# Performance work log

Hardware: AMD Instinct MI355X
Metric: run time of the kernel (lower is better)

Reference implementation:

```python
import jax, jax.numpy as jnp
import numpy as np
from jax import lax

B, C, H, W, D, V = 1, 32, 128, 160, 64, 5


def _make_projs():
    # proj_matrices[b, v, 0] = 4x4 extrinsics [R|t], proj_matrices[b, v, 1] = 4x4 intrinsics
    f = 800.0
    K = np.eye(4, dtype=np.float32)
    K[0, 0] = K[1, 1] = f
    K[0, 2] = W / 2.0
    K[1, 2] = H / 2.0
    projs = np.zeros((B, V, 2, 4, 4), np.float32)
    for b in range(B):
        for v in range(V):
            E = np.eye(4, dtype=np.float32)
            if v > 0:
                ang = 0.02 * v
                ca, sa = np.cos(ang), np.sin(ang)
                E[:3, :3] = np.array([[ca, 0.0, sa], [0.0, 1.0, 0.0], [-sa, 0.0, ca]], np.float32)
                E[:3, 3] = np.array([0.1 * v, 0.02 * v, 0.05 * v], np.float32)
            projs[b, v, 0] = E
            projs[b, v, 1] = K
    return jnp.asarray(projs)


def setup_inputs() -> dict:
    key = jax.random.key(0)
    ks = jax.random.split(key, 6)
    inp = {f"feat{i}": jax.random.normal(ks[i], (B, C, H, W), jnp.float32) for i in range(V)}
    inp["proj_matrices"] = _make_projs()
    inp["depth_values"] = jnp.broadcast_to(
        jnp.linspace(425.0, 935.0, D, dtype=jnp.float32)[None, :], (B, D))
    inp["num_depth"] = D
    inp["conv_w"] = jax.random.normal(ks[5], (1, C, 3, 3, 3), jnp.float32) * 0.05
    inp["conv_b"] = jnp.zeros((1,), jnp.float32)
    return inp


def _bilinear_sample(fea, px, py):
    # fea: [B,C,H,W]; px,py: [B,N] pixel coords. Bilinear, zero padding, align_corners=True.
    Bb, Cc, Hh, Ww = fea.shape
    fea_flat = fea.reshape(Bb, Cc, Hh * Ww)
    x0 = jnp.floor(px)
    y0 = jnp.floor(py)
    wx1 = px - x0
    wy1 = py - y0

    def corner(xc, yc, w):
        valid = (xc >= 0) & (xc <= Ww - 1) & (yc >= 0) & (yc <= Hh - 1)
        xi = jnp.clip(xc, 0, Ww - 1).astype(jnp.int32)
        yi = jnp.clip(yc, 0, Hh - 1).astype(jnp.int32)
        idx = yi * Ww + xi  # [B,N]
        g = jax.vmap(lambda fb, ib: fb[:, ib])(fea_flat, idx)  # [B,C,N]
        return g * (w * valid)[:, None, :]

    return (corner(x0, y0, (1 - wx1) * (1 - wy1))
            + corner(x0 + 1, y0, wx1 * (1 - wy1))
            + corner(x0, y0 + 1, (1 - wx1) * wy1)
            + corner(x0 + 1, y0 + 1, wx1 * wy1))


def _homo_warp(src_fea, src_proj, ref_proj, depth_values):
    # homo_warping_3D: warp src features into ref frustum at each depth hypothesis
    Bb, Cc, Hh, Ww = src_fea.shape
    Dd = depth_values.shape[1]
    proj = jnp.einsum('bij,bjk->bik', src_proj, jnp.linalg.inv(ref_proj))
    rot, trans = proj[:, :3, :3], proj[:, :3, 3]
    yy, xx = jnp.meshgrid(jnp.arange(Hh, dtype=src_fea.dtype),
                          jnp.arange(Ww, dtype=src_fea.dtype), indexing='ij')
    xyz = jnp.stack([xx.ravel(), yy.ravel(), jnp.ones(Hh * Ww, src_fea.dtype)])  # [3,HW]
    rot_xyz = jnp.einsum('bij,jn->bin', rot, xyz)  # [B,3,HW]
    pxyz = rot_xyz[:, :, None, :] * depth_values[:, None, :, None] + trans[:, :, None, None]  # [B,3,D,HW]
    px = (pxyz[:, 0] / pxyz[:, 2]).reshape(Bb, -1)
    py = (pxyz[:, 1] / pxyz[:, 2]).reshape(Bb, -1)
    return _bilinear_sample(src_fea, px, py).reshape(Bb, Cc, Dd, Hh, Ww)


def _fuse_proj(p):
    # p: [B,2,4,4] -> [B,4,4] with K[:3,:3] @ E[:3,:4] written into top 3 rows
    top = jnp.einsum('bij,bjk->bik', p[:, 1, :3, :3], p[:, 0, :3, :4])
    return p[:, 0].at[:, :3, :4].set(top)


def reference(feat0, feat1, feat2, feat3, feat4, proj_matrices, depth_values, num_depth, conv_w, conv_b):
    feats = [feat0, feat1, feat2, feat3, feat4]
    num_views = len(feats)
    Bb, Cc, Hh, Ww = feat0.shape
    ref_proj = _fuse_proj(proj_matrices[:, 0])
    ref_vol = jnp.broadcast_to(feat0[:, :, None, :, :], (Bb, Cc, num_depth, Hh, Ww))
    vol_sum = ref_vol
    vol_sq = ref_vol ** 2
    for v in range(1, num_views):
        src_proj = _fuse_proj(proj_matrices[:, v])
        warped = _homo_warp(feats[v], src_proj, ref_proj, depth_values)
        vol_sum = vol_sum + warped
        vol_sq = vol_sq + warped ** 2
    variance = vol_sq / num_views - (vol_sum / num_views) ** 2  # [B,C,D,H,W]
    cost = lax.conv_general_dilated(variance, conv_w, (1, 1, 1), 'SAME',
                                    dimension_numbers=('NCDHW', 'OIDHW', 'NCDHW'))
    cost = cost + conv_b[None, :, None, None, None]
    prob_volume_pre = cost[:, 0]  # squeeze channel -> [B,D,H,W]
    return jax.nn.softmax(prob_volume_pre, axis=1)
```

## Files before the change

### kernel.cpp

```cpp
#include <hip/hip_runtime.h>

#define H_ 128
#define W_ 160
#define C_ 32
#define D_ 64
#define HW_ (H_*W_)
#define DHW_ (D_*HW_)
#define NVIEW 5

#define TY 16
#define TX 16
#define HY 18
#define HXP 19
#define NP_ (HY*HXP)
#define PSTR 343

#define FEATT_SZ (NVIEW*HW_*C_)
#define MATS_OFF FEATT_SZ
#define A_OFF (MATS_OFF + 64)

__global__ void k_setup_mats(const float* __restrict__ proj,
                             float* __restrict__ mats)
{
    if (threadIdx.x != 0 || blockIdx.x != 0) return;
    double F[5][12];
    for (int v = 0; v < 5; ++v) {
        const float* E = proj + v*32;
        const float* K = proj + v*32 + 16;
        for (int i = 0; i < 3; ++i)
            for (int j = 0; j < 4; ++j) {
                double s = 0.0;
                for (int k = 0; k < 3; ++k)
                    s += (double)K[i*4+k] * (double)E[k*4+j];
                F[v][i*4+j] = s;
            }
    }
    const double m00=F[0][0], m01=F[0][1], m02=F[0][2],  t0x=F[0][3];
    const double m10=F[0][4], m11=F[0][5], m12=F[0][6],  t0y=F[0][7];
    const double m20=F[0][8], m21=F[0][9], m22=F[0][10], t0z=F[0][11];
    const double det = m00*(m11*m22-m12*m21) - m01*(m10*m22-m12*m20)
                     + m02*(m10*m21-m11*m20);
    const double id = 1.0/det;
    double inv[9];
    inv[0] = (m11*m22-m12*m21)*id; inv[1] = (m02*m21-m01*m22)*id; inv[2] = (m01*m12-m02*m11)*id;
    inv[3] = (m12*m20-m10*m22)*id; inv[4] = (m00*m22-m02*m20)*id; inv[5] = (m02*m10-m00*m12)*id;
    inv[6] = (m10*m21-m11*m20)*id; inv[7] = (m01*m20-m00*m21)*id; inv[8] = (m00*m11-m01*m10)*id;
    double it[3];
    it[0] = -(inv[0]*t0x + inv[1]*t0y + inv[2]*t0z);
    it[1] = -(inv[3]*t0x + inv[4]*t0y + inv[5]*t0z);
    it[2] = -(inv[6]*t0x + inv[7]*t0y + inv[8]*t0z);
    for (int v = 1; v < 5; ++v) {
        float* o = mats + (v-1)*12;
        for (int r = 0; r < 3; ++r) {
            for (int c = 0; c < 3; ++c) {
                double s = 0.0;
                for (int k = 0; k < 3; ++k) s += F[v][r*4+k]*inv[k*3+c];
                o[r*3+c] = (float)s;
            }
            double tr = F[v][r*4+3] + F[v][r*4+0]*it[0]
                      + F[v][r*4+1]*it[1] + F[v][r*4+2]*it[2];
            o[9+r] = (float)tr;
        }
    }
}

__global__ void k_transpose(const float* __restrict__ f, float* __restrict__ ft)
{
    __shared__ float tile[C_][65];
    const int pix0 = blockIdx.x * 64;
    const int tid = threadIdx.x;
    const int p  = tid & 63;
    const int ci = (tid >> 6) * 8;
#pragma unroll
    for (int i = 0; i < 8; ++i)
        tile[ci + i][p] = f[(size_t)(ci + i)*HW_ + pix0 + p];
    __syncthreads();
    const int c2 = tid & 31, pg = tid >> 5;
#pragma unroll
    for (int i = 0; i < 8; ++i) {
        int p2 = pg + i*8;
        ft[(size_t)(pix0 + p2)*C_ + c2] = tile[c2][p2];
    }
}

__global__ __launch_bounds__(256, 3) void k_var_conv(
    const float* __restrict__ featT, const float* __restrict__ mats,
    const float* __restrict__ depthv, const float* __restrict__ convw,
    float* __restrict__ A)
{
    __shared__ float var_lds[C_ * PSTR];
    const int x0 = blockIdx.x * TX;
    const int y0 = blockIdx.y * TY;
    const int bd = blockIdx.z;
    const float depth = depthv[bd];

    float cf[4][9];
#pragma unroll
    for (int v = 0; v < 4; ++v) {
        const float* mm = mats + v*12;
#pragma unroll
        for (int r = 0; r < 3; ++r) {
            cf[v][r*3+0] = mm[r*3+0]*depth;
            cf[v][r*3+1] = mm[r*3+1]*depth;
            cf[v][r*3+2] = fmaf(mm[r*3+2], depth, mm[9+r]);
        }
    }

    const int lane_c = (threadIdx.x & 7) * 4;
    const int pg     = threadIdx.x >> 3;

    for (int p = pg; p < NP_; p += 32) {
        const int hy = p / HXP;
        const int hx = p - hy*HXP;
        const int gy = y0 - 1 + hy;
        const int gx = x0 - 1 + hx;
        float var[4] = {0.f, 0.f, 0.f, 0.f};
        if (hx < (TX+2) && (unsigned)gy < (unsigned)H_ && (unsigned)gx < (unsigned)W_) {
            const float fgx = (float)gx, fgy = (float)gy;
            const int pix = gy*W_ + gx;
            float s[4], q[4];
            {
                float4 t = *reinterpret_cast<const float4*>(featT + (size_t)pix*C_ + lane_c);
                s[0]=t.x; s[1]=t.y; s[2]=t.z; s[3]=t.w;
#pragma unroll
                for (int k = 0; k < 4; ++k) q[k] = s[k]*s[k];
            }
#pragma unroll
            for (int v = 0; v < 4; ++v) {
                const float xx = fmaf(cf[v][0],fgx, fmaf(cf[v][1],fgy, cf[v][2]));
                const float yy = fmaf(cf[v][3],fgx, fmaf(cf[v][4],fgy, cf[v][5]));
                const float zz = fmaf(cf[v][6],fgx, fmaf(cf[v][7],fgy, cf[v][8]));
                const float rz = 1.0f / zz;
                const float px = xx*rz, py = yy*rz;
                const float xf = floorf(px), yf = floorf(py);
                const float wx = px - xf, wy = py - yf;
                const int xi = (int)xf, yi = (int)yf;
                const bool vx0 = (xi >=  0) & (xi <= W_-1);
                const bool vx1 = (xi >= -1) & (xi <= W_-2);
                const bool vy0 = (yi >=  0) & (yi <= H_-1);
                const bool vy1 = (yi >= -1) & (yi <= H_-2);
                const int xc0 = min(max(xi,   0), W_-1);
                const int xc1 = min(max(xi+1, 0), W_-1);
                const int yc0 = min(max(yi,   0), H_-1);
                const int yc1 = min(max(yi+1, 0), H_-1);
                const float ux = 1.f - wx, uy = 1.f - wy;
                const float w00 = (vx0 && vy0) ? ux*uy : 0.f;
                const float w10 = (vx1 && vy0) ? wx*uy : 0.f;
                const float w01 = (vx0 && vy1) ? ux*wy : 0.f;
                const float w11 = (vx1 && vy1) ? wx*wy : 0.f;
                const float* fb = featT + (size_t)(v+1)*HW_*C_ + lane_c;
                const float4 t00 = *reinterpret_cast<const float4*>(fb + (size_t)(yc0*W_+xc0)*C_);
                const float4 t10 = *reinterpret_cast<const float4*>(fb + (size_t)(yc0*W_+xc1)*C_);
                const float4 t01 = *reinterpret_cast<const float4*>(fb + (size_t)(yc1*W_+xc0)*C_);
                const float4 t11 = *reinterpret_cast<const float4*>(fb + (size_t)(yc1*W_+xc1)*C_);
                const float a00[4] = {t00.x,t00.y,t00.z,t00.w};
                const float a10[4] = {t10.x,t10.y,t10.z,t10.w};
                const float a01[4] = {t01.x,t01.y,t01.z,t01.w};
                const float a11[4] = {t11.x,t11.y,t11.z,t11.w};
#pragma unroll
                for (int k = 0; k < 4; ++k) {
                    float wv = fmaf(a00[k],w00, fmaf(a10[k],w10, fmaf(a01[k],w01, a11[k]*w11)));
                    s[k] += wv;
                    q[k] = fmaf(wv, wv, q[k]);
                }
            }
#pragma unroll
            for (int k = 0; k < 4; ++k) {
                const float sm = s[k]*0.2f;
                var[k] = q[k]*0.2f - sm*sm;
            }
        }
#pragma unroll
        for (int k = 0; k < 4; ++k)
            var_lds[(lane_c+k)*PSTR + p] = var[k];
    }
    __syncthreads();

    const int tid = threadIdx.x;
    const int oy = tid >> 4;
    const int ox = tid & 15;
    float a0 = 0.f, a1 = 0.f, a2 = 0.f;
#pragma unroll 4
    for (int cc = 0; cc < C_; ++cc) {
        const float* vrow = var_lds + cc*PSTR;
        const float* wc   = convw + cc*27;
#pragma unroll
        for (int ky = 0; ky < 3; ++ky) {
            const int base = (oy+ky)*HXP + ox;
            const float u0 = vrow[base+0];
            const float u1 = vrow[base+1];
            const float u2 = vrow[base+2];
            const float* wk = wc + ky*3;
            a0 = fmaf(u0, wk[0],  fmaf(u1, wk[1],  fmaf(u2, wk[2],  a0)));
            a1 = fmaf(u0, wk[9],  fmaf(u1, wk[10], fmaf(u2, wk[11], a1)));
            a2 = fmaf(u0, wk[18], fmaf(u1, wk[19], fmaf(u2, wk[20], a2)));
        }
    }
    const size_t o = (size_t)bd*HW_ + (size_t)(y0+oy)*W_ + (x0+ox);
    A[o]                    = a0;
    A[(size_t)DHW_ + o]     = a1;
    A[2*(size_t)DHW_ + o]   = a2;
}

__global__ void k_softmax(const float* __restrict__ A,
                          const float* __restrict__ conv_b,
                          float* __restrict__ out)
{
    const int pix = blockIdx.x*256 + threadIdx.x;
    const float bs = conv_b[0];
    float cst[D_];
#pragma unroll
    for (int d = 0; d < D_; ++d) {
        float v = A[(size_t)DHW_ + (size_t)d*HW_ + pix];
        if (d > 0)      v += A[(size_t)(d-1)*HW_ + pix];
        if (d < D_-1)   v += A[2*(size_t)DHW_ + (size_t)(d+1)*HW_ + pix];
        cst[d] = v + bs;
    }
    float m = cst[0];
#pragma unroll
    for (int d = 1; d < D_; ++d) m = fmaxf(m, cst[d]);
    float s = 0.f;
#pragma unroll
    for (int d = 0; d < D_; ++d) { cst[d] = expf(cst[d] - m); s += cst[d]; }
    const float rs = 1.0f / s;
#pragma unroll
    for (int d = 0; d < D_; ++d)
        out[(size_t)d*HW_ + pix] = cst[d]*rs;
}

extern "C" void kernel_launch(void* const* d_in, const int* in_sizes, int n_in,
                              void* d_out, int out_size, void* d_ws, size_t ws_size,
                              hipStream_t stream)
{
    const float* proj   = (const float*)d_in[5];
    const float* depth  = (const float*)d_in[6];
    const float* conv_w = (const float*)d_in[8];
    const float* conv_b = (const float*)d_in[9];

    float* ws    = (float*)d_ws;
    float* featT = ws;
    float* mats  = ws + MATS_OFF;
    float* A     = ws + A_OFF;

    k_setup_mats<<<1, 64, 0, stream>>>(proj, mats);
    for (int v = 0; v < 5; ++v)
        k_transpose<<<HW_/64, 256, 0, stream>>>((const float*)d_in[v],
                                                featT + (size_t)v*HW_*C_);
    dim3 g1(W_/TX, H_/TY, D_);
    k_var_conv<<<g1, 256, 0, stream>>>(featT, mats, depth, conv_w, A);
    k_softmax<<<HW_/256, 256, 0, stream>>>(A, conv_b, (float*)d_out);
}
```

Before: 202.8 us.

## Compute each halo pixel per thread across all channels with swizzled pixel-major LDS

The variance stage now assigns one halo pixel per thread instead of splitting channels across 8 lanes. Each thread computes projection, weights and offsets once per view and loops over all 32 channels, so the homography math is no longer repeated per channel group. The variance tile is stored pixel-major in LDS with an XOR swizzle and read as float4 in the conv stage, using conv weights pre-permuted per tap. The five transpose launches are merged into one 2D grid, and the reciprocal uses the hardware rcp. In exchange, only 324 of 256×2 thread slots do work (about 68 of 256 threads idle on the second pass), register use per thread grows, and each thread's gathers are now uncoalesced 128-byte rows.

```diff
diff --git a/kernel.cpp b/kernel.cpp
--- a/kernel.cpp
+++ b/kernel.cpp
@@ -6,23 +6,31 @@
 #define D_ 64
 #define HW_ (H_*W_)
 #define DHW_ (D_*HW_)
-#define NVIEW 5
 
 #define TY 16
 #define TX 16
-#define HY 18
-#define HXP 19
-#define NP_ (HY*HXP)
-#define PSTR 343
-
-#define FEATT_SZ (NVIEW*HW_*C_)
+#define HS 18
+#define NP_ (HS*HS)
+
+#define FEATT_SZ (5*HW_*C_)
 #define MATS_OFF FEATT_SZ
-#define A_OFF (MATS_OFF + 64)
-
-__global__ void k_setup_mats(const float* __restrict__ proj,
-                             float* __restrict__ mats)
-{
-    if (threadIdx.x != 0 || blockIdx.x != 0) return;
+#define CW2_OFF (MATS_OFF + 64)
+#define A_OFF (CW2_OFF + 960)
+
+__global__ void k_setup(const float* __restrict__ proj,
+                        const float* __restrict__ convw,
+                        float* __restrict__ mats,
+                        float* __restrict__ cw2)
+{
+    const int tid = threadIdx.x;
+    for (int i = tid; i < 864; i += 64) {
+        const int tap = i / 96;
+        const int rem = i - tap*96;
+        const int c   = rem / 3;
+        const int kd  = rem - c*3;
+        cw2[i] = convw[c*27 + kd*9 + tap];
+    }
+    if (tid != 0) return;
     double F[5][12];
     for (int v = 0; v < 5; ++v) {
         const float* E = proj + v*32;
@@ -64,8 +72,13 @@
     }
 }
 
-__global__ void k_transpose(const float* __restrict__ f, float* __restrict__ ft)
-{
+__global__ void k_transpose(const float* __restrict__ f0, const float* __restrict__ f1,
+                            const float* __restrict__ f2, const float* __restrict__ f3,
+                            const float* __restrict__ f4, float* __restrict__ ft)
+{
+    const int bv = blockIdx.y;
+    const float* f = (bv==0) ? f0 : (bv==1) ? f1 : (bv==2) ? f2 : (bv==3) ? f3 : f4;
+    float* o = ft + (size_t)bv * (HW_*C_);
     __shared__ float tile[C_][65];
     const int pix0 = blockIdx.x * 64;
     const int tid = threadIdx.x;
@@ -79,16 +92,17 @@
 #pragma unroll
     for (int i = 0; i < 8; ++i) {
         int p2 = pg + i*8;
-        ft[(size_t)(pix0 + p2)*C_ + c2] = tile[c2][p2];
+        o[(size_t)(pix0 + p2)*C_ + c2] = tile[c2][p2];
     }
 }
 
 __global__ __launch_bounds__(256, 3) void k_var_conv(
     const float* __restrict__ featT, const float* __restrict__ mats,
-    const float* __restrict__ depthv, const float* __restrict__ convw,
+    const float* __restrict__ depthv, const float* __restrict__ cw2,
     float* __restrict__ A)
 {
-    __shared__ float var_lds[C_ * PSTR];
+    __shared__ float vlds[NP_ * C_];
+    const int tid = threadIdx.x;
     const int x0 = blockIdx.x * TX;
     const int y0 = blockIdx.y * TY;
     const int bd = blockIdx.z;
@@ -106,100 +120,133 @@
         }
     }
 
-    const int lane_c = (threadIdx.x & 7) * 4;
-    const int pg     = threadIdx.x >> 3;
-
-    for (int p = pg; p < NP_; p += 32) {
-        const int hy = p / HXP;
-        const int hx = p - hy*HXP;
+    for (int p = tid; p < NP_; p += 256) {
+        const int hy = p / HS;
+        const int hx = p - hy*HS;
         const int gy = y0 - 1 + hy;
         const int gx = x0 - 1 + hx;
-        float var[4] = {0.f, 0.f, 0.f, 0.f};
-        if (hx < (TX+2) && (unsigned)gy < (unsigned)H_ && (unsigned)gx < (unsigned)W_) {
-            const float fgx = (float)gx, fgy = (float)gy;
-            const int pix = gy*W_ + gx;
-            float s[4], q[4];
+        const bool inimg = ((unsigned)gy < 128u) && ((unsigned)gx < 160u);
+        const float vp = inimg ? 1.f : 0.f;
+        const float fgx = (float)gx, fgy = (float)gy;
+        const int gyc = min(max(gy, 0), H_-1);
+        const int gxc = min(max(gx, 0), W_-1);
+        const int refoff = (gyc*W_ + gxc)*C_;
+
+        float wgt[4][4];
+        int   off[4][4];
+#pragma unroll
+        for (int v = 0; v < 4; ++v) {
+            const float xx = fmaf(cf[v][0],fgx, fmaf(cf[v][1],fgy, cf[v][2]));
+            const float yy = fmaf(cf[v][3],fgx, fmaf(cf[v][4],fgy, cf[v][5]));
+            const float zz = fmaf(cf[v][6],fgx, fmaf(cf[v][7],fgy, cf[v][8]));
+            const float rz = __builtin_amdgcn_rcpf(zz);
+            const float px = xx*rz, py = yy*rz;
+            const float xf = floorf(px), yf = floorf(py);
+            const float wx = px - xf, wy = py - yf;
+            const int xi = (int)xf, yi = (int)yf;
+            const bool vx0 = (xi >=  0) & (xi <= W_-1);
+            const bool vx1 = (xi >= -1) & (xi <= W_-2);
+            const bool vy0 = (yi >=  0) & (yi <= H_-1);
+            const bool vy1 = (yi >= -1) & (yi <= H_-2);
+            const int xc0 = min(max(xi,   0), W_-1);
+            const int xc1 = min(max(xi+1, 0), W_-1);
+            const int yr0 = min(max(yi,   0), H_-1) * W_;
+            const int yr1 = min(max(yi+1, 0), H_-1) * W_;
+            const float ux = 1.f - wx, uy = 1.f - wy;
+            wgt[v][0] = (inimg && vx0 && vy0) ? ux*uy : 0.f;
+            wgt[v][1] = (inimg && vx1 && vy0) ? wx*uy : 0.f;
+            wgt[v][2] = (inimg && vx0 && vy1) ? ux*wy : 0.f;
+            wgt[v][3] = (inimg && vx1 && vy1) ? wx*wy : 0.f;
+            off[v][0] = (yr0 + xc0)*C_;
+            off[v][1] = (yr0 + xc1)*C_;
+            off[v][2] = (yr1 + xc0)*C_;
+            off[v][3] = (yr1 + xc1)*C_;
+        }
+
+        const int sw = p & 7;
+        float* vout = vlds + p*C_;
+#pragma unroll
+        for (int cp = 0; cp < 4; ++cp) {
+            const int c0 = cp*8;
+            float s0[4], q0[4], s1[4], q1[4];
             {
-                float4 t = *reinterpret_cast<const float4*>(featT + (size_t)pix*C_ + lane_c);
-                s[0]=t.x; s[1]=t.y; s[2]=t.z; s[3]=t.w;
-#pragma unroll
-                for (int k = 0; k < 4; ++k) q[k] = s[k]*s[k];
+                const float4 t0 = *reinterpret_cast<const float4*>(featT + refoff + c0);
+                const float4 t1 = *reinterpret_cast<const float4*>(featT + refoff + c0 + 4);
+                const float t0a[4] = {t0.x,t0.y,t0.z,t0.w};
+                const float t1a[4] = {t1.x,t1.y,t1.z,t1.w};
+#pragma unroll
+                for (int k = 0; k < 4; ++k) {
+                    s0[k] = t0a[k]*vp;  q0[k] = s0[k]*t0a[k];
+                    s1[k] = t1a[k]*vp;  q1[k] = s1[k]*t1a[k];
+                }
             }
 #pragma unroll
             for (int v = 0; v < 4; ++v) {
-                const float xx = fmaf(cf[v][0],fgx, fmaf(cf[v][1],fgy, cf[v][2]));
-                const float yy = fmaf(cf[v][3],fgx, fmaf(cf[v][4],fgy, cf[v][5]));
-                const float zz = fmaf(cf[v][6],fgx, fmaf(cf[v][7],fgy, cf[v][8]));
-                const float rz = 1.0f / zz;
-                const float px = xx*rz, py = yy*rz;
-                const float xf = floorf(px), yf = floorf(py);
-                const float wx = px - xf, wy = py - yf;
-                const int xi = (int)xf, yi = (int)yf;
-                const bool vx0 = (xi >=  0) & (xi <= W_-1);
-                const bool vx1 = (xi >= -1) & (xi <= W_-2);
-                const bool vy0 = (yi >=  0) & (yi <= H_-1);
-                const bool vy1 = (yi >= -1) & (yi <= H_-2);
-                const int xc0 = min(max(xi,   0), W_-1);
-                const int xc1 = min(max(xi+1, 0), W_-1);
-                const int yc0 = min(max(yi,   0), H_-1);
-                const int yc1 = min(max(yi+1, 0), H_-1);
-                const float ux = 1.f - wx, uy = 1.f - wy;
-                const float w00 = (vx0 && vy0) ? ux*uy : 0.f;
-                const float w10 = (vx1 && vy0) ? wx*uy : 0.f;
-                const float w01 = (vx0 && vy1) ? ux*wy : 0.f;
-                const float w11 = (vx1 && vy1) ? wx*wy : 0.f;
-                const float* fb = featT + (size_t)(v+1)*HW_*C_ + lane_c;
-                const float4 t00 = *reinterpret_cast<const float4*>(fb + (size_t)(yc0*W_+xc0)*C_);
-                const float4 t10 = *reinterpret_cast<const float4*>(fb + (size_t)(yc0*W_+xc1)*C_);
-                const float4 t01 = *reinterpret_cast<const float4*>(fb + (size_t)(yc1*W_+xc0)*C_);
-                const float4 t11 = *reinterpret_cast<const float4*>(fb + (size_t)(yc1*W_+xc1)*C_);
-                const float a00[4] = {t00.x,t00.y,t00.z,t00.w};
-                const float a10[4] = {t10.x,t10.y,t10.z,t10.w};
-                const float a01[4] = {t01.x,t01.y,t01.z,t01.w};
-                const float a11[4] = {t11.x,t11.y,t11.z,t11.w};
+                const float* fb = featT + (size_t)(v+1)*(HW_*C_) + c0;
+                float4 a0c[4], a1c[4];
+#pragma unroll
+                for (int c4 = 0; c4 < 4; ++c4) {
+                    a0c[c4] = *reinterpret_cast<const float4*>(fb + off[v][c4]);
+                    a1c[c4] = *reinterpret_cast<const float4*>(fb + off[v][c4] + 4);
+                }
+                const float w0 = wgt[v][0], w1 = wgt[v][1], w2 = wgt[v][2], w3 = wgt[v][3];
+                const float a00[4]={a0c[0].x,a0c[0].y,a0c[0].z,a0c[0].w};
+                const float a10[4]={a0c[1].x,a0c[1].y,a0c[1].z,a0c[1].w};
+                const float a01[4]={a0c[2].x,a0c[2].y,a0c[2].z,a0c[2].w};
+                const float a11[4]={a0c[3].x,a0c[3].y,a0c[3].z,a0c[3].w};
+                const float b00[4]={a1c[0].x,a1c[0].y,a1c[0].z,a1c[0].w};
+                const float b10[4]={a1c[1].x,a1c[1].y,a1c[1].z,a1c[1].w};
+                const float b01[4]={a1c[2].x,a1c[2].y,a1c[2].z,a1c[2].w};
+                const float b11[4]={a1c[3].x,a1c[3].y,a1c[3].z,a1c[3].w};
 #pragma unroll
                 for (int k = 0; k < 4; ++k) {
-                    float wv = fmaf(a00[k],w00, fmaf(a10[k],w10, fmaf(a01[k],w01, a11[k]*w11)));
-                    s[k] += wv;
-                    q[k] = fmaf(wv, wv, q[k]);
+                    const float wv0 = fmaf(a00[k],w0, fmaf(a10[k],w1, fmaf(a01[k],w2, a11[k]*w3)));
+                    s0[k] += wv0;  q0[k] = fmaf(wv0, wv0, q0[k]);
+                    const float wv1 = fmaf(b00[k],w0, fmaf(b10[k],w1, fmaf(b01[k],w2, b11[k]*w3)));
+                    s1[k] += wv1;  q1[k] = fmaf(wv1, wv1, q1[k]);
                 }
             }
+            float o0[4], o1[4];
 #pragma unroll
             for (int k = 0; k < 4; ++k) {
-                const float sm = s[k]*0.2f;
-                var[k] = q[k]*0.2f - sm*sm;
-            }
-        }
-#pragma unroll
-        for (int k = 0; k < 4; ++k)
-            var_lds[(lane_c+k)*PSTR + p] = var[k];
+                const float m0 = s0[k]*0.2f;  o0[k] = q0[k]*0.2f - m0*m0;
+                const float m1 = s1[k]*0.2f;  o1[k] = q1[k]*0.2f - m1*m1;
+            }
+            *reinterpret_cast<float4*>(vout + (((2*cp  )^sw)<<2)) = make_float4(o0[0],o0[1],o0[2],o0[3]);
+            *reinterpret_cast<float4*>(vout + (((2*cp+1)^sw)<<2)) = make_float4(o1[0],o1[1],o1[2],o1[3]);
+        }
     }
     __syncthreads();
 
-    const int tid = threadIdx.x;
     const int oy = tid >> 4;
     const int ox = tid & 15;
-    float a0 = 0.f, a1 = 0.f, a2 = 0.f;
-#pragma unroll 4
-    for (int cc = 0; cc < C_; ++cc) {
-        const float* vrow = var_lds + cc*PSTR;
-        const float* wc   = convw + cc*27;
-#pragma unroll
-        for (int ky = 0; ky < 3; ++ky) {
-            const int base = (oy+ky)*HXP + ox;
-            const float u0 = vrow[base+0];
-            const float u1 = vrow[base+1];
-            const float u2 = vrow[base+2];
-            const float* wk = wc + ky*3;
-            a0 = fmaf(u0, wk[0],  fmaf(u1, wk[1],  fmaf(u2, wk[2],  a0)));
-            a1 = fmaf(u0, wk[9],  fmaf(u1, wk[10], fmaf(u2, wk[11], a1)));
-            a2 = fmaf(u0, wk[18], fmaf(u1, wk[19], fmaf(u2, wk[20], a2)));
+    float acc0 = 0.f, acc1 = 0.f, acc2 = 0.f;
+#pragma unroll
+    for (int ky = 0; ky < 3; ++ky) {
+#pragma unroll
+        for (int kx = 0; kx < 3; ++kx) {
+            const int p = (oy+ky)*HS + (ox+kx);
+            const int sw = p & 7;
+            const float* wt   = cw2 + (ky*3+kx)*96;
+            const float* vrow = vlds + p*C_;
+#pragma unroll
+            for (int cq = 0; cq < 8; ++cq) {
+                const float4 dv = *reinterpret_cast<const float4*>(vrow + ((cq^sw)<<2));
+                const float da[4] = {dv.x,dv.y,dv.z,dv.w};
+#pragma unroll
+                for (int k = 0; k < 4; ++k) {
+                    const float* wc = wt + (cq*4+k)*3;
+                    acc0 = fmaf(da[k], wc[0], acc0);
+                    acc1 = fmaf(da[k], wc[1], acc1);
+                    acc2 = fmaf(da[k], wc[2], acc2);
+                }
+            }
         }
     }
     const size_t o = (size_t)bd*HW_ + (size_t)(y0+oy)*W_ + (x0+ox);
-    A[o]                    = a0;
-    A[(size_t)DHW_ + o]     = a1;
-    A[2*(size_t)DHW_ + o]   = a2;
+    A[o]                    = acc0;
+    A[(size_t)DHW_ + o]     = acc1;
+    A[2*(size_t)DHW_ + o]   = acc2;
 }
 
 __global__ void k_softmax(const float* __restrict__ A,
@@ -240,13 +287,15 @@
     float* ws    = (float*)d_ws;
     float* featT = ws;
     float* mats  = ws + MATS_OFF;
+    float* cw2   = ws + CW2_OFF;
     float* A     = ws + A_OFF;
 
-    k_setup_mats<<<1, 64, 0, stream>>>(proj, mats);
-    for (int v = 0; v < 5; ++v)
-        k_transpose<<<HW_/64, 256, 0, stream>>>((const float*)d_in[v],
-                                                featT + (size_t)v*HW_*C_);
+    k_setup<<<1, 64, 0, stream>>>(proj, conv_w, mats, cw2);
+    dim3 gt(HW_/64, 5);
+    k_transpose<<<gt, 256, 0, stream>>>((const float*)d_in[0], (const float*)d_in[1],
+                                        (const float*)d_in[2], (const float*)d_in[3],
+                                        (const float*)d_in[4], featT);
     dim3 g1(W_/TX, H_/TY, D_);
-    k_var_conv<<<g1, 256, 0, stream>>>(featT, mats, depth, conv_w, A);
+    k_var_conv<<<g1, 256, 0, stream>>>(featT, mats, depth, cw2, A);
     k_softmax<<<HW_/256, 256, 0, stream>>>(A, conv_b, (float*)d_out);
 }
```

Result: slower. 774.0 us (+281.7%).
